# Performance work log

Hardware: AMD Instinct MI355X
Metric: run time of the kernel (lower is better)

## Reference

```python
import jax, jax.numpy as jnp
import numpy as np

N, C, H, W = 32, 1, 100, 168
STRIDE = 8
PRE_NMS_TOP_N = 1000   # pre_nms_top_n
POST_NMS_TOP_N = 100   # fpn_post_nms_top_n
PRE_NMS_THRESH = 0.01  # hardcoded in original forward_for_single_feature_map
NMS_THRESH = 0.5
MIN_SIZE = 0


def setup_inputs() -> dict:
    key = jax.random.key(0)
    k1, k2, k3 = jax.random.split(key, 3)
    # FCOS location grid at stride 8, flattened in (H, W) row-major order to match
    # permute(0,2,3,1).reshape(N,-1,...) layout of the predictions.
    xs = jnp.arange(W, dtype=jnp.float32) * STRIDE + STRIDE // 2
    ys = jnp.arange(H, dtype=jnp.float32) * STRIDE + STRIDE // 2
    xg, yg = jnp.meshgrid(xs, ys)  # (H, W); xg[h,w]=xs[w], yg[h,w]=ys[h]
    locations = jnp.stack([xg.ravel(), yg.ravel()], axis=-1)  # [H*W, 2]
    box_cls = jax.random.normal(k1, (N, C, H, W), jnp.float32) * 2.0 - 2.0
    box_regression = jax.random.uniform(k2, (N, 4, H, W), jnp.float32) * 64.0
    centerness = jax.random.normal(k3, (N, 1, H, W), jnp.float32)
    return {"locations": locations, "box_cls": box_cls,
            "box_regression": box_regression, "centerness": centerness,
            "image_h": 800, "image_w": 1344}


def _pairwise_iou(boxes):
    # boxes: [K, 4] xyxy
    x1, y1, x2, y2 = boxes[:, 0], boxes[:, 1], boxes[:, 2], boxes[:, 3]
    area = jnp.maximum(x2 - x1, 0.0) * jnp.maximum(y2 - y1, 0.0)
    iw = jnp.maximum(jnp.minimum(x2[:, None], x2[None, :]) - jnp.maximum(x1[:, None], x1[None, :]), 0.0)
    ih = jnp.maximum(jnp.minimum(y2[:, None], y2[None, :]) - jnp.maximum(y1[:, None], y1[None, :]), 0.0)
    inter = iw * ih
    union = area[:, None] + area[None, :] - inter
    return inter / jnp.maximum(union, 1e-9)


def _nms_keep(iou, valid):
    # Greedy NMS on boxes already sorted by descending score. valid marks real
    # (above-threshold, non-small) candidates; invalid boxes never suppress.
    K = valid.shape[0]
    idx = jnp.arange(K)

    def body(keep, i):
        sup = jnp.take(keep, i) & (jnp.take(iou, i, axis=0) > NMS_THRESH) & (idx > i)
        return keep & ~sup, None

    keep, _ = jax.lax.scan(body, valid, idx)
    return keep


def _single_image(scores, reg, locations, img_h, img_w):
    # scores: [H*W*C] sigmoid probs (class-major last, idx%C=class, idx//C=loc)
    # reg:    [H*W, 4] (l, t, r, b) distances
    top_scores, top_idx = jax.lax.top_k(scores, PRE_NMS_TOP_N)  # sorted desc
    loc_idx = top_idx // C
    labels = (top_idx % C + 1).astype(jnp.float32)
    valid = top_scores > PRE_NMS_THRESH  # candidate_inds = box_cls > thresh
    locs = jnp.take(locations, loc_idx, axis=0)  # [K, 2]
    r = jnp.take(reg, loc_idx, axis=0)           # [K, 4]
    # box decode + clip_to_image (TO_REMOVE=1 convention of BoxList)
    x1 = jnp.clip(locs[:, 0] - r[:, 0], 0.0, img_w - 1.0)
    y1 = jnp.clip(locs[:, 1] - r[:, 1], 0.0, img_h - 1.0)
    x2 = jnp.clip(locs[:, 0] + r[:, 2], 0.0, img_w - 1.0)
    y2 = jnp.clip(locs[:, 1] + r[:, 3], 0.0, img_h - 1.0)
    # remove_small_boxes (ws/hs with TO_REMOVE=1)
    valid = valid & ((x2 - x1 + 1.0) >= MIN_SIZE) & ((y2 - y1 + 1.0) >= MIN_SIZE)
    boxes = jnp.stack([x1, y1, x2, y2], axis=1)  # [K, 4]
    keep = _nms_keep(_pairwise_iou(boxes), valid)  # single fg class -> one NMS
    kept_scores = jnp.where(keep, top_scores, 0.0)
    # keep top fpn_post_nms_top_n by score (kthvalue threshold equivalent)
    final_scores, fi = jax.lax.top_k(kept_scores, POST_NMS_TOP_N)
    det = jnp.concatenate([jnp.take(boxes, fi, axis=0),
                           final_scores[:, None],
                           jnp.take(labels, fi)[:, None]], axis=1)  # [K_out, 6]
    return det


def reference(locations, box_cls, box_regression, centerness, image_h, image_w):
    # [N,C,H,W] -> [N, H*W*C] sigmoid scores (matches permute+reshape+sigmoid)
    scores = jax.nn.sigmoid(jnp.transpose(box_cls, (0, 2, 3, 1)).reshape(N, -1))
    reg = jnp.transpose(box_regression, (0, 2, 3, 1)).reshape(N, -1, 4)
    _ = jax.nn.sigmoid(centerness.reshape(N, -1))  # computed by original, unused in scoring
    img_h = jnp.float32(image_h)
    img_w = jnp.float32(image_w)
    det = jax.vmap(lambda s, r: _single_image(s, r, locations, img_h, img_w))(scores, reg)
    return det  # [N, POST_NMS_TOP_N, 6] = (x1,y1,x2,y2,score,label); score==0 rows are padding
```

## Files before the change

### kernel.cpp

```cpp
#include <hip/hip_runtime.h>
#include <cstdint>


typedef unsigned long long u64;
typedef unsigned int u32;

#define HW_TOT 16800
#define W_GRID 168
#define K_PRE  1000
#define NRANK  1024
#define N_IMG  32

#define SCORES_OFF 0
#define VALID_OFF  (N_IMG * NRANK * 4)
#define BOXES_OFF  (VALID_OFF + N_IMG * NRANK * 4)
#define MASK_OFF   (BOXES_OFF + N_IMG * NRANK * 16)
#define UARR_OFF   (MASK_OFF + N_IMG * NRANK * 16 * 8)
#define GHIST_OFF  (UARR_OFF + N_IMG * HW_TOT * 4)
#define WS_NEED    ((size_t)GHIST_OFF + (size_t)N_IMG * 256 * 4)

__global__ __launch_bounds__(1024) void fcos_zero(u32* __restrict__ ghist) {
  ghist[blockIdx.x * 1024 + threadIdx.x] = 0u;
}

__global__ __launch_bounds__(256) void fcos_keys(
    const float* __restrict__ box_cls, u32* __restrict__ uarr,
    u32* __restrict__ ghist)
{
  const int n = blockIdx.y, g = blockIdx.x;
  const int t = threadIdx.x;
  const int lane = t & 63;
  __shared__ u32 hist[256];
  hist[t] = 0u;
  __syncthreads();
  const int base = g * 2100;
  const float* cls = box_cls + (size_t)n * HW_TOT;
  #pragma unroll
  for (int k = 0; k < 9; ++k) {
    int i = base + k * 256 + t;
    bool ok = (i < base + 2100);
    u32 u = 0;
    if (ok) {
      float x = cls[i];
      double sd = 1.0 / (1.0 + exp(-(double)x));
      float s = (float)sd;
      u32 b = __float_as_uint(s);
      u = (b & 0x80000000u) ? ~b : (b | 0x80000000u);
      uarr[(size_t)n * HW_TOT + i] = u;
    }
    u32 bin = u >> 24;
    u64 same = __ballot(ok);
    #pragma unroll
    for (int b2 = 0; b2 < 8; ++b2) {
      u64 bb = __ballot(ok && ((bin >> b2) & 1u));
      same &= ((bin >> b2) & 1u) ? bb : ~bb;
    }
    if (ok) {
      int ldr = __ffsll((long long)same) - 1;
      if (lane == ldr) atomicAdd(&hist[bin], (u32)__popcll(same));
    }
  }
  __syncthreads();
  if (hist[t]) atomicAdd(&ghist[n * 256 + t], hist[t]);
}

__global__ __launch_bounds__(1024) void fcos_sel(
    const u32* __restrict__ uarr, const u32* __restrict__ ghist,
    const float* __restrict__ box_reg,
    const int* __restrict__ imh, const int* __restrict__ imw,
    float* __restrict__ scores_ws, u32* __restrict__ valid_ws,
    float* __restrict__ boxes_ws)
{
  const int n = blockIdx.x;
  const int t = threadIdx.x;
  const int lane = t & 63;
  __shared__ u32 hist[256];
  __shared__ u64 prefix_s;
  __shared__ u32 kneed_s, cnt_s;
  __shared__ u64 skey[1024];

  u64 kreg[17];
  const u32* uimg = uarr + (size_t)n * HW_TOT;
  #pragma unroll
  for (int k = 0; k < 17; ++k) {
    int i = t + k * 1024;
    kreg[k] = (i < HW_TOT)
        ? (((u64)uimg[i] << 16) | (u64)(0xFFFFu - (u32)i)) : 0ull;
  }
  if (t == 0) { prefix_s = 0ull; kneed_s = K_PRE; cnt_s = 0u; }

  if (t < 256) hist[t] = ghist[n * 256 + t];
  __syncthreads();
  {
    if (t < 64) {
      u32 h0 = hist[4*t], h1 = hist[4*t+1], h2 = hist[4*t+2], h3 = hist[4*t+3];
      u32 bs = h0 + h1 + h2 + h3, s = bs;
      #pragma unroll
      for (int off = 1; off < 64; off <<= 1) {
        u32 tmp = __shfl_down(s, off);
        if (t + off < 64) s += tmp;
      }
      u32 tail = s - bs;
      hist[4*t+3] = h3 + tail;
      hist[4*t+2] = h2 + h3 + tail;
      hist[4*t+1] = h1 + h2 + h3 + tail;
      hist[4*t]   = bs + tail;
    }
    __syncthreads();
    bool sel = false; u32 kn = 0, gt = 0;
    if (t < 256) {
      u32 ge = hist[t];
      gt = (t < 255) ? hist[t + 1] : 0u;
      kn = kneed_s;
      sel = (ge >= kn) && (gt < kn);
    }
    __syncthreads();
    if (sel) { prefix_s = (u64)t; kneed_s = kn - gt; }
    __syncthreads();
  }

  for (int p = 4; p >= 0; --p) {
    if (t < 256) hist[t] = 0u;
    __syncthreads();
    const u64 pref = prefix_s;
    const int sh = p * 8;
    #pragma unroll
    for (int k = 0; k < 17; ++k) {
      u64 key = kreg[k];
      bool act = ((key >> (sh + 8)) == pref);
      if (__ballot(act) != 0ull) {
        u32 bin = (u32)((key >> sh) & 0xFFull);
        u64 same = __ballot(act);
        #pragma unroll
        for (int b = 0; b < 8; ++b) {
          u64 bb = __ballot(act && ((bin >> b) & 1u));
          same &= ((bin >> b) & 1u) ? bb : ~bb;
        }
        if (act) {
          int ldr = __ffsll((long long)same) - 1;
          if (lane == ldr) atomicAdd(&hist[bin], (u32)__popcll(same));
        }
      }
    }
    __syncthreads();
    if (t < 64) {
      u32 h0 = hist[4*t], h1 = hist[4*t+1], h2 = hist[4*t+2], h3 = hist[4*t+3];
      u32 bs = h0 + h1 + h2 + h3, s = bs;
      #pragma unroll
      for (int off = 1; off < 64; off <<= 1) {
        u32 tmp = __shfl_down(s, off);
        if (t + off < 64) s += tmp;
      }
      u32 tail = s - bs;
      hist[4*t+3] = h3 + tail;
      hist[4*t+2] = h2 + h3 + tail;
      hist[4*t+1] = h1 + h2 + h3 + tail;
      hist[4*t]   = bs + tail;
    }
    __syncthreads();
    bool sel = false; u32 kn = 0, gt = 0;
    if (t < 256) {
      u32 ge = hist[t];
      gt = (t < 255) ? hist[t + 1] : 0u;
      kn = kneed_s;
      sel = (ge >= kn) && (gt < kn);
    }
    const u64 curp = prefix_s;
    __syncthreads();
    if (sel) { prefix_s = (curp << 8) | (u64)t; kneed_s = kn - gt; }
    __syncthreads();
  }

  const u64 T = prefix_s;
  skey[t] = 0ull;
  __syncthreads();
  #pragma unroll
  for (int k = 0; k < 17; ++k) {
    if (kreg[k] >= T) {
      u32 pos = atomicAdd(&cnt_s, 1u);
      if (pos < 1024u) skey[pos] = kreg[k];
    }
  }
  __syncthreads();

  u64 key = skey[t];
  #pragma unroll
  for (u32 k2 = 2; k2 <= 64; k2 <<= 1) {
    #pragma unroll
    for (u32 j = k2 >> 1; j > 0; j >>= 1) {
      u64 other = __shfl_xor(key, (int)j);
      bool takeMax = (((t & k2) == 0) == ((t & j) == 0));
      u64 mx = key > other ? key : other;
      u64 mn = key > other ? other : key;
      key = takeMax ? mx : mn;
    }
  }
  #pragma unroll
  for (u32 k2 = 128; k2 <= 1024; k2 <<= 1) {
    for (u32 j = k2 >> 1; j >= 64; j >>= 1) {
      skey[t] = key;
      __syncthreads();
      u64 other = skey[t ^ j];
      __syncthreads();
      bool takeMax = (((t & k2) == 0) == ((t & j) == 0));
      u64 mx = key > other ? key : other;
      u64 mn = key > other ? other : key;
      key = takeMax ? mx : mn;
    }
    #pragma unroll
    for (u32 j = 32; j > 0; j >>= 1) {
      u64 other = __shfl_xor(key, (int)j);
      bool takeMax = (((t & k2) == 0) == ((t & j) == 0));
      u64 mx = key > other ? key : other;
      u64 mn = key > other ? other : key;
      key = takeMax ? mx : mn;
    }
  }

  const float fw = (float)(*imw) - 1.0f;
  const float fh = (float)(*imh) - 1.0f;
  float* bx = boxes_ws + ((size_t)n * NRANK + t) * 4;
  if (t < K_PRE) {
    u32 u = (u32)(key >> 16);
    u32 b = (u & 0x80000000u) ? (u & 0x7FFFFFFFu) : ~u;
    float s = __uint_as_float(b);
    u32 idx = 0xFFFFu - (u32)(key & 0xFFFFull);
    int hh = (int)idx / W_GRID, ww = (int)idx - hh * W_GRID;
    float lx = (float)(ww * 8 + 4), ly = (float)(hh * 8 + 4);
    const float* rg = box_reg + (size_t)n * 4 * HW_TOT + idx;
    float r0 = rg[0], r1 = rg[HW_TOT], r2 = rg[2 * HW_TOT], r3 = rg[3 * HW_TOT];
    float x1 = fminf(fmaxf(lx - r0, 0.0f), fw);
    float y1 = fminf(fmaxf(ly - r1, 0.0f), fh);
    float x2 = fminf(fmaxf(lx + r2, 0.0f), fw);
    float y2 = fminf(fmaxf(ly + r3, 0.0f), fh);
    bool valid = (s > 0.01f) && ((x2 - x1 + 1.0f) >= 0.0f)
                             && ((y2 - y1 + 1.0f) >= 0.0f);
    scores_ws[n * NRANK + t] = s;
    valid_ws[n * NRANK + t] = valid ? 1u : 0u;
    bx[0] = x1; bx[1] = y1; bx[2] = x2; bx[3] = y2;
  } else {
    scores_ws[n * NRANK + t] = 0.0f;
    valid_ws[n * NRANK + t] = 0u;
    bx[0] = 0.0f; bx[1] = 0.0f; bx[2] = 0.0f; bx[3] = 0.0f;
  }
}

__global__ __launch_bounds__(1024) void fcos_mask(
    const float* __restrict__ boxes_ws, u64* __restrict__ mask_ws)
{
  const int n = blockIdx.y, g = blockIdx.x;
  const int t = threadIdx.x;
  __shared__ float4 bx[1024];
  bx[t] = ((const float4*)boxes_ws)[(size_t)n * NRANK + t];
  __syncthreads();
  const int wv = t >> 6, lane = t & 63;

  float4 bj[16]; float aj[16];
  #pragma unroll
  for (int c = 0; c < 16; ++c) {
    bj[c] = bx[c * 64 + lane];
    aj[c] = __fmul_rn(fmaxf(bj[c].z - bj[c].x, 0.0f), fmaxf(bj[c].w - bj[c].y, 0.0f));
  }

  u64* mimg = mask_ws + (size_t)n * NRANK * 16;
  for (int r = wv; r < 125; r += 16) {
    const int i = r * 8 + g;
    const float4 bi = bx[i];
    const float ai = __fmul_rn(fmaxf(bi.z - bi.x, 0.0f), fmaxf(bi.w - bi.y, 0.0f));
    const int cmax = i >> 6;
    #pragma unroll
    for (int c = 0; c < 16; ++c) {
      if (c <= cmax) {
        float iw  = fmaxf(fminf(bi.z, bj[c].z) - fmaxf(bi.x, bj[c].x), 0.0f);
        float ih2 = fmaxf(fminf(bi.w, bj[c].w) - fmaxf(bi.y, bj[c].y), 0.0f);
        float inter = __fmul_rn(iw, ih2);
        float uni = fmaxf(__fsub_rn(__fadd_rn(ai, aj[c]), inter), 1e-9f);
        float iou = inter / uni;
        u64 m = __ballot(iou > 0.5f);
        if (lane == 0) mimg[(size_t)i * 16 + c] = m;
      }
    }
  }
}

__global__ __launch_bounds__(64) void fcos_scan(
    const float* __restrict__ scores_ws, const u32* __restrict__ valid_ws,
    const float* __restrict__ boxes_ws, const u64* __restrict__ mask_ws,
    float* __restrict__ out)
{
  const int n = blockIdx.x;
  const int lane = threadIdx.x;
  const u64* mbase = mask_ws + (size_t)n * NRANK * 16;

  u64 vw[16];
  #pragma unroll
  for (int w = 0; w < 16; ++w)
    vw[w] = __ballot(valid_ws[n * NRANK + w * 64 + lane] != 0u);

  u64 keptw[16];
  #pragma unroll
  for (int w = 0; w < 16; ++w) keptw[w] = 0ull;

  ulonglong2 A2[8], B2[8];
#define WORD(ARR, w) ((w) & 1 ? ARR[(w) >> 1].y : ARR[(w) >> 1].x)
#define LOADBLK(DST, BLK) do { \
    const ulonglong2* _p = (const ulonglong2*)(mbase + (((size_t)(BLK)) * 64 + (size_t)lane) * 16); \
    _Pragma("unroll") \
    for (int _r = 0; _r < 8; ++_r) DST[_r] = _p[_r]; \
  } while (0)
#define PROCBLK(ARR, BV) do { \
    u64 _acc = 0ull; \
    _Pragma("unroll") \
    for (int _w = 0; _w < 16; ++_w) \
      if (_w < (BV)) _acc |= WORD(ARR, _w) & keptw[_w]; \
    u64 _live = vw[(BV)] & ~__ballot(_acc != 0ull); \
    const u64 _intra = WORD(ARR, (BV)); \
    u64 _kb = 0ull; \
    while (_live) { \
      u32 _i = (u32)(__ffsll((long long)_live) - 1); \
      _kb |= (1ull << _i); \
      u64 _sup = __ballot(((_intra >> _i) & 1ull) != 0ull); \
      _live &= ~(_sup | (1ull << _i)); \
    } \
    keptw[(BV)] = _kb; \
  } while (0)

  LOADBLK(A2, 0);
  LOADBLK(B2, 1);   PROCBLK(A2, 0);
  LOADBLK(A2, 2);   PROCBLK(B2, 1);
  LOADBLK(B2, 3);   PROCBLK(A2, 2);
  LOADBLK(A2, 4);   PROCBLK(B2, 3);
  LOADBLK(B2, 5);   PROCBLK(A2, 4);
  LOADBLK(A2, 6);   PROCBLK(B2, 5);
  LOADBLK(B2, 7);   PROCBLK(A2, 6);
  LOADBLK(A2, 8);   PROCBLK(B2, 7);
  LOADBLK(B2, 9);   PROCBLK(A2, 8);
  LOADBLK(A2, 10);  PROCBLK(B2, 9);
  LOADBLK(B2, 11);  PROCBLK(A2, 10);
  LOADBLK(A2, 12);  PROCBLK(B2, 11);
  LOADBLK(B2, 13);  PROCBLK(A2, 12);
  LOADBLK(A2, 14);  PROCBLK(B2, 13);
  LOADBLK(B2, 15);  PROCBLK(A2, 14);
                    PROCBLK(B2, 15);
#undef PROCBLK
#undef LOADBLK
#undef WORD

  __shared__ u64 kw_s[16];
  __shared__ u32 cumk_s[17], cumn_s[17];
  if (lane == 0) {
    #pragma unroll
    for (int w = 0; w < 16; ++w) kw_s[w] = keptw[w];
  }
  __syncthreads();
  if (lane == 0) {
    u32 ck = 0, cn = 0;
    for (int w = 0; w < 16; ++w) {
      cumk_s[w] = ck; cumn_s[w] = cn;
      u64 rm = (w == 15) ? ((1ull << 40) - 1ull) : ~0ull;
      ck += (u32)__popcll(kw_s[w] & rm);
      cn += (u32)__popcll(~kw_s[w] & rm);
    }
    cumk_s[16] = ck; cumn_s[16] = cn;
  }
  __syncthreads();
  const u32 mtot = cumk_s[16];

  for (int s = lane; s < 100; s += 64) {
    u32 r; float sc;
    if ((u32)s < mtot) {
      int w = 0;
      #pragma unroll
      for (int x = 1; x < 16; ++x) if (cumk_s[x] <= (u32)s) w = x;
      u64 rm = (w == 15) ? ((1ull << 40) - 1ull) : ~0ull;
      u64 word = kw_s[w] & rm;
      u32 b = (u32)s - cumk_s[w];
      for (u32 z = 0; z < b; ++z) word &= word - 1;
      r = (u32)(w * 64) + (u32)(__ffsll((long long)word) - 1);
      sc = scores_ws[n * NRANK + r];
    } else {
      u32 s2 = (u32)s - mtot;
      int w = 0;
      #pragma unroll
      for (int x = 1; x < 16; ++x) if (cumn_s[x] <= s2) w = x;
      u64 rm = (w == 15) ? ((1ull << 40) - 1ull) : ~0ull;
      u64 word = (~kw_s[w]) & rm;
      u32 b = s2 - cumn_s[w];
      for (u32 z = 0; z < b; ++z) word &= word - 1;
      r = (u32)(w * 64) + (u32)(__ffsll((long long)word) - 1);
      sc = 0.0f;
    }
    const float* bxp = boxes_ws + ((size_t)n * NRANK + r) * 4;
    float* o = out + ((size_t)n * 100 + s) * 6;
    o[0] = bxp[0]; o[1] = bxp[1]; o[2] = bxp[2]; o[3] = bxp[3];
    o[4] = sc; o[5] = 1.0f;
  }
}

extern "C" void kernel_launch(void* const* d_in, const int* in_sizes, int n_in,
                              void* d_out, int out_size, void* d_ws, size_t ws_size,
                              hipStream_t stream) {
  (void)in_sizes; (void)n_in; (void)out_size;
  if (ws_size < WS_NEED) return;

  const float* box_cls = (const float*)d_in[1];
  const float* box_reg = (const float*)d_in[2];
  const int* imh = (const int*)d_in[4];
  const int* imw = (const int*)d_in[5];

  char* ws = (char*)d_ws;
  float* scores_ws = (float*)(ws + SCORES_OFF);
  u32*   valid_ws  = (u32*)(ws + VALID_OFF);
  float* boxes_ws  = (float*)(ws + BOXES_OFF);
  u64*   mask_ws   = (u64*)(ws + MASK_OFF);
  u32*   uarr_ws   = (u32*)(ws + UARR_OFF);
  u32*   ghist_ws  = (u32*)(ws + GHIST_OFF);
  float* out = (float*)d_out;

  fcos_zero<<<8, 1024, 0, stream>>>(ghist_ws);
  dim3 gK(8, N_IMG);
  fcos_keys<<<gK, 256, 0, stream>>>(box_cls, uarr_ws, ghist_ws);
  fcos_sel<<<N_IMG, 1024, 0, stream>>>(uarr_ws, ghist_ws, box_reg, imh, imw,
                                       scores_ws, valid_ws, boxes_ws);
  dim3 gB(8, N_IMG);
  fcos_mask<<<gB, 1024, 0, stream>>>(boxes_ws, mask_ws);
  fcos_scan<<<N_IMG, 64, 0, stream>>>(scores_ws, valid_ws, boxes_ws, mask_ws, out);
}
```

Baseline: 171.7 us.

## Replace bitonic sort with rank-count selection and shrink radix passes to 32-bit keys

The top-k selection now radix-selects on 32-bit score keys, which takes three refinement passes instead of five 64-bit ones. Ties at the threshold are resolved by index rank, and the 1000 candidates are ordered by O(K^2) rank counting instead of a 1024-wide bitonic sort with many block barriers. The keys kernel is spread over 32 blocks per image instead of 8 to raise parallelism. The rank counting trades barrier-heavy sorting for more shared-memory reads per thread, and the tie handling adds an extra quadratic loop when many scores are equal.

```diff
diff --git a/kernel.cpp b/kernel.cpp
--- a/kernel.cpp
+++ b/kernel.cpp
@@ -33,31 +33,34 @@
   __shared__ u32 hist[256];
   hist[t] = 0u;
   __syncthreads();
-  const int base = g * 2100;
+  const int base = g * 525;
   const float* cls = box_cls + (size_t)n * HW_TOT;
   #pragma unroll
-  for (int k = 0; k < 9; ++k) {
-    int i = base + k * 256 + t;
-    bool ok = (i < base + 2100);
+  for (int k = 0; k < 3; ++k) {
+    int loc = k * 256 + t;
+    bool ok = (loc < 525);
     u32 u = 0;
     if (ok) {
-      float x = cls[i];
+      float x = cls[base + loc];
       double sd = 1.0 / (1.0 + exp(-(double)x));
       float s = (float)sd;
       u32 b = __float_as_uint(s);
       u = (b & 0x80000000u) ? ~b : (b | 0x80000000u);
-      uarr[(size_t)n * HW_TOT + i] = u;
+      uarr[(size_t)n * HW_TOT + base + loc] = u;
     }
     u32 bin = u >> 24;
-    u64 same = __ballot(ok);
-    #pragma unroll
-    for (int b2 = 0; b2 < 8; ++b2) {
-      u64 bb = __ballot(ok && ((bin >> b2) & 1u));
-      same &= ((bin >> b2) & 1u) ? bb : ~bb;
-    }
-    if (ok) {
-      int ldr = __ffsll((long long)same) - 1;
-      if (lane == ldr) atomicAdd(&hist[bin], (u32)__popcll(same));
+    u64 ba = __ballot(ok);
+    if (ba) {
+      u64 same = ba;
+      #pragma unroll
+      for (int b2 = 0; b2 < 8; ++b2) {
+        u64 bb = __ballot(ok && ((bin >> b2) & 1u));
+        same &= ((bin >> b2) & 1u) ? bb : ~bb;
+      }
+      if (ok) {
+        int ldr = __ffsll((long long)same) - 1;
+        if (lane == ldr) atomicAdd(&hist[bin], (u32)__popcll(same));
+      }
     }
   }
   __syncthreads();
@@ -75,22 +78,22 @@
   const int t = threadIdx.x;
   const int lane = t & 63;
   __shared__ u32 hist[256];
-  __shared__ u64 prefix_s;
-  __shared__ u32 kneed_s, cnt_s;
-  __shared__ u64 skey[1024];
-
-  u64 kreg[17];
+  __shared__ u32 prefix_s, kneed_s, cab_s, tie_s;
+  __shared__ u64 cand[1024];
+  __shared__ u64 ord[1024];
+  __shared__ u32 tieidx[1024];
+
+  u32 kreg[17];
   const u32* uimg = uarr + (size_t)n * HW_TOT;
   #pragma unroll
   for (int k = 0; k < 17; ++k) {
     int i = t + k * 1024;
-    kreg[k] = (i < HW_TOT)
-        ? (((u64)uimg[i] << 16) | (u64)(0xFFFFu - (u32)i)) : 0ull;
-  }
-  if (t == 0) { prefix_s = 0ull; kneed_s = K_PRE; cnt_s = 0u; }
-
+    kreg[k] = (i < HW_TOT) ? uimg[i] : 0u;
+  }
+  if (t == 0) { prefix_s = 0u; kneed_s = K_PRE; cab_s = 0u; tie_s = 0u; }
   if (t < 256) hist[t] = ghist[n * 256 + t];
   __syncthreads();
+
   {
     if (t < 64) {
       u32 h0 = hist[4*t], h1 = hist[4*t+1], h2 = hist[4*t+2], h3 = hist[4*t+3];
@@ -115,22 +118,23 @@
       sel = (ge >= kn) && (gt < kn);
     }
     __syncthreads();
-    if (sel) { prefix_s = (u64)t; kneed_s = kn - gt; }
-    __syncthreads();
-  }
-
-  for (int p = 4; p >= 0; --p) {
+    if (sel) { prefix_s = (u32)t; kneed_s = kn - gt; }
+    __syncthreads();
+  }
+
+  for (int p = 2; p >= 0; --p) {
     if (t < 256) hist[t] = 0u;
     __syncthreads();
-    const u64 pref = prefix_s;
-    const int sh = p * 8;
+    const u32 pref = prefix_s;
+    const int shA = (p + 1) * 8, shB = p * 8;
     #pragma unroll
     for (int k = 0; k < 17; ++k) {
-      u64 key = kreg[k];
-      bool act = ((key >> (sh + 8)) == pref);
-      if (__ballot(act) != 0ull) {
-        u32 bin = (u32)((key >> sh) & 0xFFull);
-        u64 same = __ballot(act);
+      u32 u = kreg[k];
+      bool act = ((u >> shA) == pref);
+      u64 ba = __ballot(act);
+      if (ba) {
+        u32 bin = (u >> shB) & 0xFFu;
+        u64 same = ba;
         #pragma unroll
         for (int b = 0; b < 8; ++b) {
           u64 bb = __ballot(act && ((bin >> b) & 1u));
@@ -165,62 +169,54 @@
       kn = kneed_s;
       sel = (ge >= kn) && (gt < kn);
     }
-    const u64 curp = prefix_s;
-    __syncthreads();
-    if (sel) { prefix_s = (curp << 8) | (u64)t; kneed_s = kn - gt; }
-    __syncthreads();
-  }
-
-  const u64 T = prefix_s;
-  skey[t] = 0ull;
-  __syncthreads();
+    const u32 curp = prefix_s;
+    __syncthreads();
+    if (sel) { prefix_s = (curp << 8) | (u32)t; kneed_s = kn - gt; }
+    __syncthreads();
+  }
+
+  const u32 T32 = prefix_s;
   #pragma unroll
   for (int k = 0; k < 17; ++k) {
-    if (kreg[k] >= T) {
-      u32 pos = atomicAdd(&cnt_s, 1u);
-      if (pos < 1024u) skey[pos] = kreg[k];
-    }
-  }
-  __syncthreads();
-
-  u64 key = skey[t];
-  #pragma unroll
-  for (u32 k2 = 2; k2 <= 64; k2 <<= 1) {
-    #pragma unroll
-    for (u32 j = k2 >> 1; j > 0; j >>= 1) {
-      u64 other = __shfl_xor(key, (int)j);
-      bool takeMax = (((t & k2) == 0) == ((t & j) == 0));
-      u64 mx = key > other ? key : other;
-      u64 mn = key > other ? other : key;
-      key = takeMax ? mx : mn;
-    }
-  }
-  #pragma unroll
-  for (u32 k2 = 128; k2 <= 1024; k2 <<= 1) {
-    for (u32 j = k2 >> 1; j >= 64; j >>= 1) {
-      skey[t] = key;
-      __syncthreads();
-      u64 other = skey[t ^ j];
-      __syncthreads();
-      bool takeMax = (((t & k2) == 0) == ((t & j) == 0));
-      u64 mx = key > other ? key : other;
-      u64 mn = key > other ? other : key;
-      key = takeMax ? mx : mn;
-    }
-    #pragma unroll
-    for (u32 j = 32; j > 0; j >>= 1) {
-      u64 other = __shfl_xor(key, (int)j);
-      bool takeMax = (((t & k2) == 0) == ((t & j) == 0));
-      u64 mx = key > other ? key : other;
-      u64 mn = key > other ? other : key;
-      key = takeMax ? mx : mn;
-    }
-  }
+    int i = t + k * 1024;
+    u32 u = kreg[k];
+    if (u > T32) {
+      u32 pos = atomicAdd(&cab_s, 1u);
+      cand[pos] = ((u64)u << 16) | (u64)(0xFFFFu - (u32)i);
+    } else if (u == T32) {
+      u32 tp = atomicAdd(&tie_s, 1u);
+      if (tp < 1024u) tieidx[tp] = (u32)i;
+    }
+  }
+  __syncthreads();
+  const u32 c1 = cab_s, tcnt = tie_s, need_t = (u32)K_PRE - c1;
+  for (u32 j = t; j < tcnt; j += 1024) {
+    u32 idx = tieidx[j];
+    u32 rk = 0;
+    for (u32 m = 0; m < tcnt; ++m) rk += (tieidx[m] < idx) ? 1u : 0u;
+    if (rk < need_t)
+      cand[c1 + rk] = ((u64)T32 << 16) | (u64)(0xFFFFu - idx);
+  }
+  __syncthreads();
+
+  if (t < K_PRE) {
+    u64 kt = cand[t];
+    u32 rk = 0;
+    const ulonglong2* c2 = (const ulonglong2*)cand;
+    for (int j = 0; j < K_PRE / 2; ++j) {
+      ulonglong2 v = c2[j];
+      rk += (v.x > kt) ? 1u : 0u;
+      rk += (v.y > kt) ? 1u : 0u;
+    }
+    ord[rk] = kt;
+  }
+  __syncthreads();
 
   const float fw = (float)(*imw) - 1.0f;
   const float fh = (float)(*imh) - 1.0f;
   float* bx = boxes_ws + ((size_t)n * NRANK + t) * 4;
   if (t < K_PRE) {
+    u64 key = ord[t];
     u32 u = (u32)(key >> 16);
     u32 b = (u & 0x80000000u) ? (u & 0x7FFFFFFFu) : ~u;
     float s = __uint_as_float(b);
@@ -418,7 +414,7 @@
   float* out = (float*)d_out;
 
   fcos_zero<<<8, 1024, 0, stream>>>(ghist_ws);
-  dim3 gK(8, N_IMG);
+  dim3 gK(32, N_IMG);
   fcos_keys<<<gK, 256, 0, stream>>>(box_cls, uarr_ws, ghist_ws);
   fcos_sel<<<N_IMG, 1024, 0, stream>>>(uarr_ws, ghist_ws, box_reg, imh, imw,
                                        scores_ws, valid_ws, boxes_ws);
```

New measurement: 177.6 us. 1.03x slower.
